# Performance work log

Hardware: AMD Instinct MI355X
Metric: run time of the kernel (lower is better)

The kernel has to match this reference:

```python
import jax, jax.numpy as jnp
import numpy as np

N_NODES = 6144
IN_FEATURES = 256
N_HEADS = 4
N_HIDDEN = 64  # out_features, concat=False
LEAKY_SLOPE = 0.2
NEG_INF = -9e16


def setup_inputs() -> dict:
    key = jax.random.key(0)
    k1, k2, k3, k4 = jax.random.split(key, 4)
    h = jax.random.normal(k1, (N_NODES, IN_FEATURES), dtype=jnp.float32)
    adj_mat = jax.random.randint(k2, (N_NODES, N_NODES), 0, 2, dtype=jnp.int32)
    W = jax.random.normal(k3, (IN_FEATURES, N_HEADS * N_HIDDEN), dtype=jnp.float32) * 0.06
    a = jax.random.normal(k4, (N_HEADS, 2 * N_HIDDEN, 1), dtype=jnp.float32) * 0.1
    return {"h": h, "adj_mat": adj_mat, "W": W, "a": a}


def reference(h, adj_mat, W, a):
    n_nodes = h.shape[0]
    # linear transform, dropout is identity in eval mode
    ht = (h @ W).reshape(n_nodes, N_HEADS, N_HIDDEN).transpose(1, 0, 2)  # [H, N, d]
    a_src = a[:, :N_HIDDEN, 0]   # [H, d]
    a_tgt = a[:, N_HIDDEN:, 0]   # [H, d]
    src = jnp.einsum('hnd,hd->hn', ht, a_src)  # [H, N]
    tgt = jnp.einsum('hnd,hd->hn', ht, a_tgt)  # [H, N]
    e = src[:, :, None] + tgt[:, None, :]       # [H, N, N]
    e = jnp.where(e >= 0, e, LEAKY_SLOPE * e)    # leaky relu
    e = jnp.where(adj_mat[None, :, :] > 0, e, jnp.float32(NEG_INF))
    attention = jax.nn.softmax(e, axis=-1)       # [H, N, N]
    h_prime = jnp.einsum('hij,hjd->hid', attention, ht)  # [H, N, d]
    return h_prime.mean(axis=0)                  # [N, d] (concat=False)
```

## Files before the change

### kernel.cpp

```cpp
#include <hip/hip_runtime.h>
#include <hip/hip_bf16.h>

#define N_NODES 6144
#define IN_F 256
#define N_HEADS 4
#define N_HID 64
#define NWORDS (N_NODES / 32)
#define JS 8
#define JLEN (N_NODES / JS)
#define NW (JLEN / 32)
#define SM_STRIDE 28

typedef __attribute__((ext_vector_type(4))) float floatx4;
typedef _Float16 half2_t __attribute__((ext_vector_type(2)));
typedef _Float16 half8_t __attribute__((ext_vector_type(8)));
typedef __attribute__((ext_vector_type(4))) unsigned uint4_t;
typedef short short2v __attribute__((ext_vector_type(2)));

__global__ __launch_bounds__(256) void pack_adj_kernel(
    const int* __restrict__ adj, unsigned* __restrict__ mask32)
{
    const int waveId = (blockIdx.x * 256 + threadIdx.x) >> 6;
    const int lane = threadIdx.x & 63;
    #pragma unroll
    for (int c = 0; c < 3; ++c) {
        const size_t W = ((size_t)c * 6144 + waveId) * 64 + lane;
        const int* p = adj + W * 32;
        unsigned mw = 0;
        #pragma unroll
        for (int k = 0; k < 8; ++k) {
            const int4 v = *(const int4*)(p + k * 4);
            mw |= (unsigned)v.x << (k * 4 + 0);
            mw |= (unsigned)v.y << (k * 4 + 1);
            mw |= (unsigned)v.z << (k * 4 + 2);
            mw |= (unsigned)v.w << (k * 4 + 3);
        }
        mask32[W] = mw;
    }
}

__global__ __launch_bounds__(256) void ht_gemm_kernel(
    const float* __restrict__ h, const float* __restrict__ W,
    const float* __restrict__ a, short* __restrict__ htF,
    float* __restrict__ srcv, unsigned* __restrict__ tE1pk, unsigned* __restrict__ tE2pk)
{
    __shared__ float As[32][34];
    __shared__ float Bs[32][68];
    __shared__ float redS[32][16];
    __shared__ float redT[32][16];
    __shared__ unsigned short eh1[32], eh2[32];

    const int head = blockIdx.y;
    const int i0 = blockIdx.x * 32;
    const int tid = threadIdx.x;
    const int tx = tid & 15, ty = tid >> 4;

    float acc[2][4] = {};

    for (int k0 = 0; k0 < IN_F; k0 += 32) {
        __syncthreads();
        {
            const int m = tid >> 3, kq = tid & 7;
            const float4 v = *(const float4*)(h + (i0 + m) * IN_F + k0 + kq * 4);
            As[kq*4+0][m] = v.x; As[kq*4+1][m] = v.y;
            As[kq*4+2][m] = v.z; As[kq*4+3][m] = v.w;
        }
        #pragma unroll
        for (int it = 0; it < 2; ++it) {
            int l = it * 256 + tid;
            int k = l >> 4, nq = l & 15;
            *(float4*)&Bs[k][nq*4] = *(const float4*)(W + (k0 + k) * 256 + head * 64 + nq * 4);
        }
        __syncthreads();
        #pragma unroll
        for (int kk = 0; kk < 32; ++kk) {
            const float2 av = *(const float2*)&As[kk][ty*2];
            const float4 bv = *(const float4*)&Bs[kk][tx*4];
            const float aa[2] = {av.x, av.y};
            const float bb[4] = {bv.x, bv.y, bv.z, bv.w};
            #pragma unroll
            for (int r = 0; r < 2; ++r)
                #pragma unroll
                for (int c = 0; c < 4; ++c)
                    acc[r][c] = fmaf(aa[r], bb[c], acc[r][c]);
        }
    }

    #pragma unroll
    for (int r = 0; r < 2; ++r)
        #pragma unroll
        for (int c2 = 0; c2 < 4; ++c2) {
            const int d = tx * 4 + c2;
            const int j = i0 + ty * 2 + r;
            const int jt = j >> 5, q = (j >> 3) & 3, u = j & 7;
            const int c = d >> 4, n = d & 15;
            const size_t F = (((((size_t)head * 192 + jt) * 4 + c) * 16 + n) * 4 + q) * 8 + u;
            const _Float16 hv = (_Float16)acc[r][c2];
            htF[F] = *(const short*)&hv;
        }

    float as_[4], at_[4];
    #pragma unroll
    for (int c = 0; c < 4; ++c) {
        as_[c] = a[head * 128 + tx * 4 + c];
        at_[c] = a[head * 128 + 64 + tx * 4 + c];
    }
    #pragma unroll
    for (int r = 0; r < 2; ++r) {
        float ps = 0.f, pt = 0.f;
        #pragma unroll
        for (int c = 0; c < 4; ++c) {
            ps = fmaf(acc[r][c], as_[c], ps);
            pt = fmaf(acc[r][c], at_[c], pt);
        }
        redS[ty*2+r][tx] = ps;
        redT[ty*2+r][tx] = pt;
    }
    __syncthreads();
    if (tid < 64) {
        const int row = tid & 31;
        const float* src = (tid < 32) ? &redS[row][0] : &redT[row][0];
        float s = 0.f;
        #pragma unroll
        for (int x = 0; x < 16; ++x) s += src[x];
        if (tid < 32) {
            srcv[head * N_NODES + i0 + row] = s;
        } else {
            const _Float16 E1 = (_Float16)__expf(s);
            const _Float16 E2 = (_Float16)__expf(0.2f * s);
            eh1[row] = *(const unsigned short*)&E1;
            eh2[row] = *(const unsigned short*)&E2;
        }
    }
    __syncthreads();
    if (tid < 16) {
        const unsigned v1 = (unsigned)eh1[2*tid] | ((unsigned)eh1[2*tid+1] << 16);
        const unsigned v2 = (unsigned)eh2[2*tid] | ((unsigned)eh2[2*tid+1] << 16);
        tE1pk[head * (N_NODES/2) + i0/2 + tid] = v1;
        tE2pk[head * (N_NODES/2) + i0/2 + tid] = v2;
    }
}

__global__ __launch_bounds__(256, 3) void gat_main_kernel(
    const unsigned* __restrict__ mask32, const short* __restrict__ htF,
    const float* __restrict__ srcv, const unsigned* __restrict__ tE1pk,
    const unsigned* __restrict__ tE2pk,
    float* __restrict__ pnum, float* __restrict__ pden)
{
    __shared__ unsigned smask[256 * SM_STRIDE];
    __shared__ uint4_t sE1v[96], sE2v[96];

    const int lane = threadIdx.x;
    const int wy = threadIdx.y;
    const int jc = blockIdx.y;
    const int head = blockIdx.z;
    const int rb0 = blockIdx.x * 256;
    const int m = lane & 15, quad = lane >> 4;
    const int jbase = jc * JLEN;

    const int tid = wy * 64 + lane;
    #pragma unroll
    for (int it = 0; it < 6; ++it) {
        const int flat = it * 256 + tid;
        const int r = flat / 6, w4 = flat % 6;
        const uint4_t v = *(const uint4_t*)(mask32 + (size_t)(rb0 + r) * NWORDS + jc * NW + w4 * 4);
        *(uint4_t*)&smask[r * SM_STRIDE + w4 * 4] = v;
    }
    if (tid < 192) {
        const unsigned* g = (tid < 96)
            ? (tE1pk + head * (N_NODES/2) + (jbase >> 1) + tid * 4)
            : (tE2pk + head * (N_NODES/2) + (jbase >> 1) + (tid - 96) * 4);
        const uint4_t v = *(const uint4_t*)g;
        if (tid < 96) sE1v[tid] = v; else sE2v[tid - 96] = v;
    }
    __syncthreads();

    const int rowbase = rb0 + wy * 64;
    half2_t e1s[4], e2s[4];
    #pragma unroll
    for (int t = 0; t < 4; ++t) {
        const float sv = srcv[head * N_NODES + rowbase + t * 16 + m];
        const _Float16 a1 = (_Float16)__expf(sv);
        const _Float16 a2 = (_Float16)__expf(0.2f * sv);
        e1s[t] = (half2_t){a1, a1};
        e2s[t] = (half2_t){a2, a2};
    }

    const short* fb = htF + ((size_t)(head * 192 + (jbase >> 5)) * 4) * 512 + (m * 4 + quad) * 8;
    const unsigned* mrow = &smask[(wy * 64 + m) * SM_STRIDE];

    half8_t bones;
    #pragma unroll
    for (int u = 0; u < 8; ++u) bones[u] = (_Float16)1.0f;

    floatx4 accN[4][4];
    floatx4 accD[4];
    #pragma unroll
    for (int t = 0; t < 4; ++t) {
        accD[t] = (floatx4){0,0,0,0};
        #pragma unroll
        for (int c = 0; c < 4; ++c) accN[t][c] = (floatx4){0,0,0,0};
    }

    half8_t bn[4];
    #pragma unroll
    for (int c = 0; c < 4; ++c) bn[c] = *(const half8_t*)(fb + c * 512);

    for (int w = 0; w < NW; ++w) {
        half8_t bc[4];
        #pragma unroll
        for (int c = 0; c < 4; ++c) bc[c] = bn[c];
        const int wn = (w + 1 < NW) ? (w + 1) : w;
        #pragma unroll
        for (int c = 0; c < 4; ++c)
            bn[c] = *(const half8_t*)(fb + (size_t)wn * 2048 + c * 512);

        const uint4_t E1 = sE1v[w * 4 + quad];
        const uint4_t E2 = sE2v[w * 4 + quad];
        const unsigned E1a[4] = {E1.x, E1.y, E1.z, E1.w};
        const unsigned E2a[4] = {E2.x, E2.y, E2.z, E2.w};

        #pragma unroll
        for (int t = 0; t < 4; ++t) {
            const unsigned bits = (mrow[t * (16*SM_STRIDE) + w] >> (quad * 8)) & 0xffu;
            const short2v tt = __builtin_bit_cast(short2v, bits * 0x10001u);
            uint4_t af_u;
            #pragma unroll
            for (int p = 0; p < 4; ++p) {
                const short2v shl = (p == 0) ? (short2v){15,14} : (p == 1) ? (short2v){13,12}
                                 : (p == 2) ? (short2v){11,10} : (short2v){9,8};
                const short2v k = (tt << shl) >> (short2v){15,15};
                const half2_t p1 = __builtin_bit_cast(half2_t, E1a[p]) * e1s[t];
                const half2_t p2 = __builtin_bit_cast(half2_t, E2a[p]) * e2s[t];
                const half2_t mx = __builtin_elementwise_max(p1, p2);
                const unsigned r = __builtin_bit_cast(unsigned, mx) & __builtin_bit_cast(unsigned, k);
                if (p == 0) af_u.x = r; else if (p == 1) af_u.y = r;
                else if (p == 2) af_u.z = r; else af_u.w = r;
            }
            const half8_t af = __builtin_bit_cast(half8_t, af_u);
            #pragma unroll
            for (int c = 0; c < 4; ++c)
                accN[t][c] = __builtin_amdgcn_mfma_f32_16x16x32_f16(af, bc[c], accN[t][c], 0, 0, 0);
            accD[t] = __builtin_amdgcn_mfma_f32_16x16x32_f16(af, bones, accD[t], 0, 0, 0);
        }
    }

    const int slot = jc * N_HEADS + head;
    #pragma unroll
    for (int t = 0; t < 4; ++t) {
        if (m == 0) {
            #pragma unroll
            for (int r = 0; r < 4; ++r)
                pden[slot * N_NODES + rowbase + t * 16 + quad * 4 + r] = accD[t][r];
        }
        #pragma unroll
        for (int r = 0; r < 4; ++r) {
            const int gi = rowbase + t * 16 + quad * 4 + r;
            float* np_ = pnum + ((size_t)slot * N_NODES + gi) * N_HID + m;
            np_[0]  = accN[t][0][r];
            np_[16] = accN[t][1][r];
            np_[32] = accN[t][2][r];
            np_[48] = accN[t][3][r];
        }
    }
}

__global__ __launch_bounds__(256) void finalize_kernel(
    const float* __restrict__ pnum, const float* __restrict__ pden,
    float* __restrict__ out)
{
    const int idx = blockIdx.x * 256 + threadIdx.x;
    if (idx >= N_NODES * N_HID) return;
    const int i = idx >> 6;
    const int d = idx & 63;
    float s = 0.f;
    #pragma unroll
    for (int hh = 0; hh < N_HEADS; ++hh) {
        float ns = 0.f, ds = 0.f;
        #pragma unroll
        for (int jc = 0; jc < JS; ++jc) {
            const int slot = jc * N_HEADS + hh;
            ns += pnum[((size_t)slot * N_NODES + i) * N_HID + d];
            ds += pden[slot * N_NODES + i];
        }
        s += ns / ds;
    }
    out[idx] = 0.25f * s;
}

extern "C" void kernel_launch(void* const* d_in, const int* in_sizes, int n_in,
                              void* d_out, int out_size, void* d_ws, size_t ws_size,
                              hipStream_t stream)
{
    const float* h   = (const float*)d_in[0];
    const int*   adj = (const int*)d_in[1];
    const float* W   = (const float*)d_in[2];
    const float* a   = (const float*)d_in[3];
    float* out = (float*)d_out;

    char* ws = (char*)d_ws;
    short* htF = (short*)ws;
    size_t off = (size_t)N_HEADS * N_HID * N_NODES * 2;
    float* srcv = (float*)(ws + off);        off += (size_t)N_HEADS * N_NODES * 4;
    unsigned* tE1pk = (unsigned*)(ws + off); off += (size_t)N_HEADS * (N_NODES/2) * 4;
    unsigned* tE2pk = (unsigned*)(ws + off); off += (size_t)N_HEADS * (N_NODES/2) * 4;
    unsigned* mask32 = (unsigned*)(ws + off); off += (size_t)N_NODES * NWORDS * 4;
    float* pnum = (float*)(ws + off);        off += (size_t)JS * N_HEADS * N_NODES * N_HID * 4;
    float* pden = (float*)(ws + off);

    pack_adj_kernel<<<1536, 256, 0, stream>>>(adj, mask32);
    ht_gemm_kernel<<<dim3(N_NODES / 32, N_HEADS), 256, 0, stream>>>(h, W, a, htF, srcv, tE1pk, tE2pk);
    gat_main_kernel<<<dim3(N_NODES / 256, JS, N_HEADS), dim3(64, 4), 0, stream>>>(
        mask32, htF, srcv, tE1pk, tE2pk, pnum, pden);
    finalize_kernel<<<dim3((N_NODES * N_HID) / 256), 256, 0, stream>>>(pnum, pden, out);
}
```

Before: 280.0 us.

## Transpose shared mask layout, fully unroll main loop, vectorize finalize

```diff
diff --git a/kernel.cpp b/kernel.cpp
--- a/kernel.cpp
+++ b/kernel.cpp
@@ -9,7 +9,7 @@
 #define JS 8
 #define JLEN (N_NODES / JS)
 #define NW (JLEN / 32)
-#define SM_STRIDE 28
+#define SMT_STRIDE 100
 
 typedef __attribute__((ext_vector_type(4))) float floatx4;
 typedef _Float16 half2_t __attribute__((ext_vector_type(2)));
@@ -147,7 +147,7 @@
     const unsigned* __restrict__ tE2pk,
     float* __restrict__ pnum, float* __restrict__ pden)
 {
-    __shared__ unsigned smask[256 * SM_STRIDE];
+    __shared__ unsigned smask[4 * 16 * SMT_STRIDE];
     __shared__ uint4_t sE1v[96], sE2v[96];
 
     const int lane = threadIdx.x;
@@ -157,14 +157,19 @@
     const int rb0 = blockIdx.x * 256;
     const int m = lane & 15, quad = lane >> 4;
     const int jbase = jc * JLEN;
-
     const int tid = wy * 64 + lane;
+
     #pragma unroll
     for (int it = 0; it < 6; ++it) {
         const int flat = it * 256 + tid;
         const int r = flat / 6, w4 = flat % 6;
         const uint4_t v = *(const uint4_t*)(mask32 + (size_t)(rb0 + r) * NWORDS + jc * NW + w4 * 4);
-        *(uint4_t*)&smask[r * SM_STRIDE + w4 * 4] = v;
+        const int wyr = r >> 6, tt = (r >> 4) & 3, mm = r & 15;
+        unsigned* base = &smask[(wyr * 16 + mm) * SMT_STRIDE + tt];
+        base[(w4 * 4 + 0) * 4] = v.x;
+        base[(w4 * 4 + 1) * 4] = v.y;
+        base[(w4 * 4 + 2) * 4] = v.z;
+        base[(w4 * 4 + 3) * 4] = v.w;
     }
     if (tid < 192) {
         const unsigned* g = (tid < 96)
@@ -187,7 +192,7 @@
     }
 
     const short* fb = htF + ((size_t)(head * 192 + (jbase >> 5)) * 4) * 512 + (m * 4 + quad) * 8;
-    const unsigned* mrow = &smask[(wy * 64 + m) * SM_STRIDE];
+    const unsigned* mrow = &smask[(wy * 16 + m) * SMT_STRIDE];
 
     half8_t bones;
     #pragma unroll
@@ -202,27 +207,23 @@
         for (int c = 0; c < 4; ++c) accN[t][c] = (floatx4){0,0,0,0};
     }
 
-    half8_t bn[4];
-    #pragma unroll
-    for (int c = 0; c < 4; ++c) bn[c] = *(const half8_t*)(fb + c * 512);
-
+    #pragma unroll
     for (int w = 0; w < NW; ++w) {
-        half8_t bc[4];
-        #pragma unroll
-        for (int c = 0; c < 4; ++c) bc[c] = bn[c];
-        const int wn = (w + 1 < NW) ? (w + 1) : w;
+        half8_t b[4];
         #pragma unroll
         for (int c = 0; c < 4; ++c)
-            bn[c] = *(const half8_t*)(fb + (size_t)wn * 2048 + c * 512);
-
+            b[c] = *(const half8_t*)(fb + (size_t)w * 2048 + c * 512);
+
+        const uint4_t mq = *(const uint4_t*)(mrow + w * 4);
         const uint4_t E1 = sE1v[w * 4 + quad];
         const uint4_t E2 = sE2v[w * 4 + quad];
+        const unsigned mqa[4] = {mq.x, mq.y, mq.z, mq.w};
         const unsigned E1a[4] = {E1.x, E1.y, E1.z, E1.w};
         const unsigned E2a[4] = {E2.x, E2.y, E2.z, E2.w};
 
         #pragma unroll
         for (int t = 0; t < 4; ++t) {
-            const unsigned bits = (mrow[t * (16*SM_STRIDE) + w] >> (quad * 8)) & 0xffu;
+            const unsigned bits = (mqa[t] >> (quad * 8)) & 0xffu;
             const short2v tt = __builtin_bit_cast(short2v, bits * 0x10001u);
             uint4_t af_u;
             #pragma unroll
@@ -240,7 +241,7 @@
             const half8_t af = __builtin_bit_cast(half8_t, af_u);
             #pragma unroll
             for (int c = 0; c < 4; ++c)
-                accN[t][c] = __builtin_amdgcn_mfma_f32_16x16x32_f16(af, bc[c], accN[t][c], 0, 0, 0);
+                accN[t][c] = __builtin_amdgcn_mfma_f32_16x16x32_f16(af, b[c], accN[t][c], 0, 0, 0);
             accD[t] = __builtin_amdgcn_mfma_f32_16x16x32_f16(af, bones, accD[t], 0, 0, 0);
         }
     }
@@ -270,22 +271,25 @@
     float* __restrict__ out)
 {
     const int idx = blockIdx.x * 256 + threadIdx.x;
-    if (idx >= N_NODES * N_HID) return;
-    const int i = idx >> 6;
-    const int d = idx & 63;
-    float s = 0.f;
+    if (idx >= N_NODES * 16) return;
+    const int i = idx >> 4;
+    const int d4 = (idx & 15) * 4;
+    float sx = 0.f, sy = 0.f, sz = 0.f, sw = 0.f;
     #pragma unroll
     for (int hh = 0; hh < N_HEADS; ++hh) {
-        float ns = 0.f, ds = 0.f;
+        float nx = 0.f, ny = 0.f, nz = 0.f, nw_ = 0.f, ds = 0.f;
         #pragma unroll
         for (int jc = 0; jc < JS; ++jc) {
             const int slot = jc * N_HEADS + hh;
-            ns += pnum[((size_t)slot * N_NODES + i) * N_HID + d];
+            const float4 v = *(const float4*)(pnum + ((size_t)slot * N_NODES + i) * N_HID + d4);
+            nx += v.x; ny += v.y; nz += v.z; nw_ += v.w;
             ds += pden[slot * N_NODES + i];
         }
-        s += ns / ds;
-    }
-    out[idx] = 0.25f * s;
+        const float r = 1.0f / ds;
+        sx += nx * r; sy += ny * r; sz += nz * r; sw += nw_ * r;
+    }
+    float4 o; o.x = 0.25f * sx; o.y = 0.25f * sy; o.z = 0.25f * sz; o.w = 0.25f * sw;
+    *(float4*)(out + (size_t)i * N_HID + d4) = o;
 }
 
 extern "C" void kernel_launch(void* const* d_in, const int* in_sizes, int n_in,
@@ -312,5 +316,5 @@
     ht_gemm_kernel<<<dim3(N_NODES / 32, N_HEADS), 256, 0, stream>>>(h, W, a, htF, srcv, tE1pk, tE2pk);
     gat_main_kernel<<<dim3(N_NODES / 256, JS, N_HEADS), dim3(64, 4), 0, stream>>>(
         mask32, htF, srcv, tE1pk, tE2pk, pnum, pden);
-    finalize_kernel<<<dim3((N_NODES * N_HID) / 256), 256, 0, stream>>>(pnum, pden, out);
-}
+    finalize_kernel<<<dim3((N_NODES * 16 + 255) / 256), 256, 0, stream>>>(pnum, pden, out);
+}
```

Measured after the change: 313.0 us. +11.8%, slower.
